# Performance work log

Hardware: AMD Instinct MI355X
Metric: run time of the kernel (lower is better)

## Reference

```python
import jax, jax.numpy as jnp
import numpy as np

FACTOR = 2
DIM = 3
F3 = FACTOR ** DIM            # 8
B = 2                          # batch size
S = 128                        # cubic spatial shape (spatial_shape = [S, S, S])
N = 262144                     # number of active voxels
C = 32                         # feature channels
MAXS = (S + FACTOR - 1) // FACTOR  # 64, downsampled grid extent per dim
# OFFSET per torch code: cumprod of MAX reversed, reversed, + [1]
OFFSET = (MAXS ** 3, MAXS ** 2, MAXS, 1)


def setup_inputs() -> dict:
    rng = np.random.default_rng(0)
    # unique voxel coords: sample N distinct cells from the B x S^3 grid
    lin = rng.permutation(B * S ** 3)[:N].astype(np.int64)
    b = lin // (S ** 3)
    r = lin % (S ** 3)
    x = r // (S * S)
    y = (r // S) % S
    z = r % S
    coords = jnp.asarray(np.stack([b, x, y, z], axis=-1), dtype=jnp.int32)  # [N, 4]
    feats = jax.random.normal(jax.random.key(0), (N, C), dtype=jnp.float32)
    return {"feats": feats, "coords": coords}


def reference(feats, coords):
    c = coords.astype(jnp.int32)
    down = c[:, 1:] // FACTOR          # [N, 3] downsampled spatial coords
    sub = c[:, 1:] % FACTOR            # [N, 3] position within factor^3 cell
    # subidx = sum(sub[..., i] * factor**i), i=0 -> x
    subidx = sub[:, 0] + sub[:, 1] * FACTOR + sub[:, 2] * (FACTOR ** 2)
    # linear code over (batch, dx, dy, dz)
    code = (c[:, 0] * OFFSET[0] + down[:, 0] * OFFSET[1]
            + down[:, 1] * OFFSET[2] + down[:, 2] * OFFSET[3])
    # unique with static size=N (M_unique <= N); pad with out-of-range sentinel
    code_u, idx = jnp.unique(code, return_inverse=True, size=N,
                             fill_value=B * MAXS ** 3)
    idx = idx.reshape(-1)
    new_coords = jnp.stack(
        [code_u // OFFSET[0]]
        + [(code_u // OFFSET[i + 1]) % MAXS for i in range(DIM)], axis=-1)
    # scatter feats into channel-expanded buffer; padded rows stay zero
    buf = jnp.zeros((N * F3, C), dtype=feats.dtype).at[idx * F3 + subidx].set(feats)
    new_feats = buf.reshape(N, F3 * C)   # [N_pad, factor^3 * C]
    return new_feats, new_coords
```

## Files before the change

### kernel.cpp

```cpp
#include <hip/hip_runtime.h>

typedef unsigned int u32;
typedef float __attribute__((ext_vector_type(4))) f4;
typedef unsigned int __attribute__((ext_vector_type(4))) u4;

static constexpr u32 NCODES = 524288u;
static constexpr u32 ZB = 1024u;
static constexpr u32 TAG = 0xFFFFFFFFu;

__device__ __forceinline__ u32 code_of(int4 c) {
  return ((u32)c.x << 18) + ((u32)(c.y >> 1) << 12) +
         ((u32)(c.z >> 1) << 6) + (u32)(c.w >> 1);
}

__device__ __forceinline__ void zero_n(f4* __restrict__ base, u32 zb, u32 t, u32 cnt) {
  const f4 z = {0.f, 0.f, 0.f, 0.f};
  for (u32 i = zb * 256u + t; i < cnt; i += ZB * 256u)
    __builtin_nontemporal_store(z, base + i);
}

__global__ void k_1(const int4* __restrict__ coords, u32* __restrict__ mark, u32 n,
                    f4* __restrict__ outc4, f4* __restrict__ zbase, u32 zcnt) {
  u32 b = blockIdx.x, t = threadIdx.x;
  u32 mb = n / 256u, sb = n / 1024u;
  if (b < mb) {
    mark[code_of(coords[b * 256u + t])] = TAG;
  } else if (b < mb + sb) {
    u32 i = (b - mb) * 256u + t;
    const f4 s4 = {2.f, 0.f, 0.f, 0.f};
    u32 span = sb * 256u;
    for (u32 k = 0; k < 4u; ++k)
      __builtin_nontemporal_store(s4, outc4 + i + k * span);
  } else {
    zero_n(zbase, b - mb - sb, t, zcnt);
  }
}

__global__ void k_2(const u4* __restrict__ mark, u32* __restrict__ bsum,
                    f4* __restrict__ zbase, u32 zcnt) {
  u32 b = blockIdx.x, t = threadIdx.x;
  if (b >= 512u) { zero_n(zbase, b - 512u, t, zcnt); return; }
  u4 m = mark[b * 256u + t];
  u32 s = (m.x == TAG) + (m.y == TAG) + (m.z == TAG) + (m.w == TAG);
  for (int d = 32; d > 0; d >>= 1) s += __shfl_down(s, d, 64);
  __shared__ u32 ws4[4];
  if ((t & 63u) == 0u) ws4[t >> 6] = s;
  __syncthreads();
  if (t == 0) bsum[b] = ws4[0] + ws4[1] + ws4[2] + ws4[3];
}

__device__ __forceinline__ void wrc(float* __restrict__ outc, u32 r, u32 code) {
  f4 p = {(float)(code >> 18), (float)((code >> 12) & 63u),
          (float)((code >> 6) & 63u), (float)(code & 63u)};
  __builtin_nontemporal_store(p, (f4*)outc + r);
}

__global__ void k_3(u32* __restrict__ codes, const u32* __restrict__ bsum,
                    float* __restrict__ outc, f4* __restrict__ zbase, u32 zcnt) {
  u32 b = blockIdx.x, t = threadIdx.x;
  if (b >= 512u) { zero_n(zbase, b - 512u, t, zcnt); return; }

  u32 v0 = bsum[t], v1 = bsum[t + 256u];
  u32 s = (t < b ? v0 : 0u) + (t + 256u < b ? v1 : 0u);
  for (int d = 32; d > 0; d >>= 1) s += __shfl_down(s, d, 64);
  __shared__ u32 ws4[4];
  if ((t & 63u) == 0u) ws4[t >> 6] = s;
  __syncthreads();
  u32 boff = ws4[0] + ws4[1] + ws4[2] + ws4[3];

  u4 m = ((const u4*)codes)[b * 256u + t];
  u32 p0 = (m.x == TAG), p1 = (m.y == TAG), p2 = (m.z == TAG), p3 = (m.w == TAG);
  u32 tsum = p0 + p1 + p2 + p3;
  u32 incl = tsum;
  u32 lane = t & 63u;
  for (int d = 1; d < 64; d <<= 1) {
    u32 v = __shfl_up(incl, d, 64);
    if (lane >= (u32)d) incl += v;
  }
  __shared__ u32 wsum[4];
  if (lane == 63u) wsum[t >> 6] = incl;
  __syncthreads();
  u32 woff = boff;
  for (u32 w = 0; w < (t >> 6); ++w) woff += wsum[w];
  u32 e0 = woff + incl - tsum;
  u32 e1 = e0 + p0, e2 = e1 + p1, e3 = e2 + p2;
  u4 r = {e0, e1, e2, e3};
  ((u4*)codes)[b * 256u + t] = r;
  u32 base = b * 1024u + t * 4u;
  if (p0) wrc(outc, e0, base + 0u);
  if (p1) wrc(outc, e1, base + 1u);
  if (p2) wrc(outc, e2, base + 2u);
  if (p3) wrc(outc, e3, base + 3u);
}

__global__ void k_4(const f4* __restrict__ feats, const int4* __restrict__ coords,
                    const u32* __restrict__ rank, f4* __restrict__ out, u32 n8) {
  u32 tid = blockIdx.x * 256u + threadIdx.x;
  if (tid >= n8) return;
  u32 row = tid >> 3, q = tid & 7u;
  int4 c = coords[row];
  u32 code = code_of(c);
  u32 sub = (u32)(c.y & 1) + ((u32)(c.z & 1) << 1) + ((u32)(c.w & 1) << 2);
  f4 f = __builtin_nontemporal_load(feats + tid);
  __builtin_nontemporal_store(f, out + ((size_t)rank[code] * 8u + sub) * 8u + q);
}

extern "C" void kernel_launch(void* const* d_in, const int* in_sizes, int n_in,
                              void* d_out, int out_size, void* d_ws, size_t ws_size,
                              hipStream_t stream) {
  const float* feats = (const float*)d_in[0];
  const int* coords  = (const int*)d_in[1];
  u32 n = (u32)(in_sizes[1] / 4);
  f4* out4 = (f4*)d_out;
  float* outc = (float*)d_out + (size_t)n * 256u;

  u32* codes = (u32*)d_ws;
  u32* bsum  = codes + NCODES;

  u32 feats4 = n * 64u;
  u32 c1 = feats4 / 3u;
  u32 c2 = c1;
  u32 c3 = feats4 - 2u * c1;
  u32 mb = n / 256u, sb = n / 1024u;

  k_1<<<mb + sb + ZB, 256, 0, stream>>>((const int4*)coords, codes, n,
                                        (f4*)outc, out4, c1);
  k_2<<<512u + ZB, 256, 0, stream>>>((const u4*)codes, bsum, out4 + c1, c2);
  k_3<<<512u + ZB, 256, 0, stream>>>(codes, bsum, outc, out4 + c1 + c2, c3);
  k_4<<<(n * 8u) / 256u, 256, 0, stream>>>((const f4*)feats, (const int4*)coords,
                                           codes, out4, n * 8u);
}
```

Measured before the change: 318.0 us.

## Fuse the four pipeline kernels into one cooperative kernel with grid syncs

Replaces the four separate launches (mark, block count, scan/emit coords, scatter) with a single cooperative kernel. Inside it, grid.sync() separates the phases, and the output zero-fill is split into thirds interleaved with the first three phases. The aim is to remove kernel launch gaps and tail effects between stages. In exchange, the grid is limited to 1024 resident blocks with grid-stride loops, and each phase now pays a grid-wide barrier. The launch also depends on every block being co-resident under the 4-blocks-per-CU bound.

```diff
diff --git a/kernel.cpp b/kernel.cpp
--- a/kernel.cpp
+++ b/kernel.cpp
@@ -1,11 +1,13 @@
 #include <hip/hip_runtime.h>
+#include <hip/hip_cooperative_groups.h>
+
+namespace cg = cooperative_groups;
 
 typedef unsigned int u32;
 typedef float __attribute__((ext_vector_type(4))) f4;
 typedef unsigned int __attribute__((ext_vector_type(4))) u4;
 
 static constexpr u32 NCODES = 524288u;
-static constexpr u32 ZB = 1024u;
 static constexpr u32 TAG = 0xFFFFFFFFu;
 
 __device__ __forceinline__ u32 code_of(int4 c) {
@@ -13,120 +15,114 @@
          ((u32)(c.z >> 1) << 6) + (u32)(c.w >> 1);
 }
 
-__device__ __forceinline__ void zero_n(f4* __restrict__ base, u32 zb, u32 t, u32 cnt) {
+__device__ __forceinline__ void zero_span(f4* __restrict__ base, u32 lo, u32 hi,
+                                          u32 gtid, u32 gt) {
   const f4 z = {0.f, 0.f, 0.f, 0.f};
-  for (u32 i = zb * 256u + t; i < cnt; i += ZB * 256u)
+  for (u32 i = lo + gtid; i < hi; i += gt)
     __builtin_nontemporal_store(z, base + i);
 }
 
-__global__ void k_1(const int4* __restrict__ coords, u32* __restrict__ mark, u32 n,
-                    f4* __restrict__ outc4, f4* __restrict__ zbase, u32 zcnt) {
+__global__ __launch_bounds__(256, 4)
+void k_all(const int4* __restrict__ coords, const f4* __restrict__ feats,
+           f4* __restrict__ out4, u32* __restrict__ codes, u32* __restrict__ bsum,
+           u32 n) {
+  cg::grid_group grid = cg::this_grid();
   u32 b = blockIdx.x, t = threadIdx.x;
-  u32 mb = n / 256u, sb = n / 1024u;
-  if (b < mb) {
-    mark[code_of(coords[b * 256u + t])] = TAG;
-  } else if (b < mb + sb) {
-    u32 i = (b - mb) * 256u + t;
-    const f4 s4 = {2.f, 0.f, 0.f, 0.f};
-    u32 span = sb * 256u;
-    for (u32 k = 0; k < 4u; ++k)
-      __builtin_nontemporal_store(s4, outc4 + i + k * span);
-  } else {
-    zero_n(zbase, b - mb - sb, t, zcnt);
+  u32 gt = gridDim.x * 256u, gtid = b * 256u + t;
+  f4* outc4 = out4 + (size_t)n * 64u;
+  u32 total4 = n * 64u;
+  u32 zc = total4 / 3u;
+
+  __shared__ u32 ws4[4];
+  __shared__ u32 wsum[4];
+
+  for (u32 i = gtid; i < n; i += gt)
+    codes[code_of(coords[i])] = TAG;
+  const f4 s4 = {2.f, 0.f, 0.f, 0.f};
+  for (u32 i = gtid; i < n; i += gt)
+    __builtin_nontemporal_store(s4, outc4 + i);
+  zero_span(out4, 0u, zc, gtid, gt);
+  grid.sync();
+
+  if (b < 512u) {
+    u4 m = ((const u4*)codes)[b * 256u + t];
+    u32 s = (m.x == TAG) + (m.y == TAG) + (m.z == TAG) + (m.w == TAG);
+    for (int d = 32; d > 0; d >>= 1) s += __shfl_down(s, d, 64);
+    if ((t & 63u) == 0u) ws4[t >> 6] = s;
+    __syncthreads();
+    if (t == 0) bsum[b] = ws4[0] + ws4[1] + ws4[2] + ws4[3];
   }
-}
+  zero_span(out4, zc, 2u * zc, gtid, gt);
+  grid.sync();
 
-__global__ void k_2(const u4* __restrict__ mark, u32* __restrict__ bsum,
-                    f4* __restrict__ zbase, u32 zcnt) {
-  u32 b = blockIdx.x, t = threadIdx.x;
-  if (b >= 512u) { zero_n(zbase, b - 512u, t, zcnt); return; }
-  u4 m = mark[b * 256u + t];
-  u32 s = (m.x == TAG) + (m.y == TAG) + (m.z == TAG) + (m.w == TAG);
-  for (int d = 32; d > 0; d >>= 1) s += __shfl_down(s, d, 64);
-  __shared__ u32 ws4[4];
-  if ((t & 63u) == 0u) ws4[t >> 6] = s;
-  __syncthreads();
-  if (t == 0) bsum[b] = ws4[0] + ws4[1] + ws4[2] + ws4[3];
-}
+  if (b < 512u) {
+    u32 v0 = bsum[t], v1 = bsum[t + 256u];
+    u32 s = (t < b ? v0 : 0u) + (t + 256u < b ? v1 : 0u);
+    for (int d = 32; d > 0; d >>= 1) s += __shfl_down(s, d, 64);
+    if ((t & 63u) == 0u) ws4[t >> 6] = s;
+    __syncthreads();
+    u32 boff = ws4[0] + ws4[1] + ws4[2] + ws4[3];
 
-__device__ __forceinline__ void wrc(float* __restrict__ outc, u32 r, u32 code) {
-  f4 p = {(float)(code >> 18), (float)((code >> 12) & 63u),
-          (float)((code >> 6) & 63u), (float)(code & 63u)};
-  __builtin_nontemporal_store(p, (f4*)outc + r);
-}
+    u4 m = ((const u4*)codes)[b * 256u + t];
+    u32 p0 = (m.x == TAG), p1 = (m.y == TAG), p2 = (m.z == TAG), p3 = (m.w == TAG);
+    u32 tsum = p0 + p1 + p2 + p3;
+    u32 incl = tsum;
+    u32 lane = t & 63u;
+    for (int d = 1; d < 64; d <<= 1) {
+      u32 v = __shfl_up(incl, d, 64);
+      if (lane >= (u32)d) incl += v;
+    }
+    if (lane == 63u) wsum[t >> 6] = incl;
+    __syncthreads();
+    u32 woff = boff;
+    for (u32 w = 0; w < (t >> 6); ++w) woff += wsum[w];
+    u32 e0 = woff + incl - tsum;
+    u32 e1 = e0 + p0, e2 = e1 + p1, e3 = e2 + p2;
+    u4 r = {e0, e1, e2, e3};
+    ((u4*)codes)[b * 256u + t] = r;
+    u32 base = b * 1024u + t * 4u;
+    if (p0) { f4 p = {(float)(base >> 18), (float)(((base + 0u) >> 12) & 63u),
+                      (float)(((base + 0u) >> 6) & 63u), (float)((base + 0u) & 63u)};
+              __builtin_nontemporal_store(p, outc4 + e0); }
+    if (p1) { u32 cd = base + 1u;
+              f4 p = {(float)(cd >> 18), (float)((cd >> 12) & 63u),
+                      (float)((cd >> 6) & 63u), (float)(cd & 63u)};
+              __builtin_nontemporal_store(p, outc4 + e1); }
+    if (p2) { u32 cd = base + 2u;
+              f4 p = {(float)(cd >> 18), (float)((cd >> 12) & 63u),
+                      (float)((cd >> 6) & 63u), (float)(cd & 63u)};
+              __builtin_nontemporal_store(p, outc4 + e2); }
+    if (p3) { u32 cd = base + 3u;
+              f4 p = {(float)(cd >> 18), (float)((cd >> 12) & 63u),
+                      (float)((cd >> 6) & 63u), (float)(cd & 63u)};
+              __builtin_nontemporal_store(p, outc4 + e3); }
+  }
+  zero_span(out4, 2u * zc, total4, gtid, gt);
+  grid.sync();
 
-__global__ void k_3(u32* __restrict__ codes, const u32* __restrict__ bsum,
-                    float* __restrict__ outc, f4* __restrict__ zbase, u32 zcnt) {
-  u32 b = blockIdx.x, t = threadIdx.x;
-  if (b >= 512u) { zero_n(zbase, b - 512u, t, zcnt); return; }
-
-  u32 v0 = bsum[t], v1 = bsum[t + 256u];
-  u32 s = (t < b ? v0 : 0u) + (t + 256u < b ? v1 : 0u);
-  for (int d = 32; d > 0; d >>= 1) s += __shfl_down(s, d, 64);
-  __shared__ u32 ws4[4];
-  if ((t & 63u) == 0u) ws4[t >> 6] = s;
-  __syncthreads();
-  u32 boff = ws4[0] + ws4[1] + ws4[2] + ws4[3];
-
-  u4 m = ((const u4*)codes)[b * 256u + t];
-  u32 p0 = (m.x == TAG), p1 = (m.y == TAG), p2 = (m.z == TAG), p3 = (m.w == TAG);
-  u32 tsum = p0 + p1 + p2 + p3;
-  u32 incl = tsum;
-  u32 lane = t & 63u;
-  for (int d = 1; d < 64; d <<= 1) {
-    u32 v = __shfl_up(incl, d, 64);
-    if (lane >= (u32)d) incl += v;
+  u32 n8 = n * 8u;
+  for (u32 i = gtid; i < n8; i += gt) {
+    u32 row = i >> 3, q = i & 7u;
+    int4 c = coords[row];
+    u32 code = code_of(c);
+    u32 sub = (u32)(c.y & 1) + ((u32)(c.z & 1) << 1) + ((u32)(c.w & 1) << 2);
+    f4 f = __builtin_nontemporal_load(feats + i);
+    __builtin_nontemporal_store(f, out4 + ((size_t)codes[code] * 8u + sub) * 8u + q);
   }
-  __shared__ u32 wsum[4];
-  if (lane == 63u) wsum[t >> 6] = incl;
-  __syncthreads();
-  u32 woff = boff;
-  for (u32 w = 0; w < (t >> 6); ++w) woff += wsum[w];
-  u32 e0 = woff + incl - tsum;
-  u32 e1 = e0 + p0, e2 = e1 + p1, e3 = e2 + p2;
-  u4 r = {e0, e1, e2, e3};
-  ((u4*)codes)[b * 256u + t] = r;
-  u32 base = b * 1024u + t * 4u;
-  if (p0) wrc(outc, e0, base + 0u);
-  if (p1) wrc(outc, e1, base + 1u);
-  if (p2) wrc(outc, e2, base + 2u);
-  if (p3) wrc(outc, e3, base + 3u);
-}
-
-__global__ void k_4(const f4* __restrict__ feats, const int4* __restrict__ coords,
-                    const u32* __restrict__ rank, f4* __restrict__ out, u32 n8) {
-  u32 tid = blockIdx.x * 256u + threadIdx.x;
-  if (tid >= n8) return;
-  u32 row = tid >> 3, q = tid & 7u;
-  int4 c = coords[row];
-  u32 code = code_of(c);
-  u32 sub = (u32)(c.y & 1) + ((u32)(c.z & 1) << 1) + ((u32)(c.w & 1) << 2);
-  f4 f = __builtin_nontemporal_load(feats + tid);
-  __builtin_nontemporal_store(f, out + ((size_t)rank[code] * 8u + sub) * 8u + q);
 }
 
 extern "C" void kernel_launch(void* const* d_in, const int* in_sizes, int n_in,
                               void* d_out, int out_size, void* d_ws, size_t ws_size,
                               hipStream_t stream) {
-  const float* feats = (const float*)d_in[0];
-  const int* coords  = (const int*)d_in[1];
+  const int4* coords = (const int4*)d_in[1];
+  const f4* feats    = (const f4*)d_in[0];
   u32 n = (u32)(in_sizes[1] / 4);
   f4* out4 = (f4*)d_out;
-  float* outc = (float*)d_out + (size_t)n * 256u;
 
   u32* codes = (u32*)d_ws;
   u32* bsum  = codes + NCODES;
 
-  u32 feats4 = n * 64u;
-  u32 c1 = feats4 / 3u;
-  u32 c2 = c1;
-  u32 c3 = feats4 - 2u * c1;
-  u32 mb = n / 256u, sb = n / 1024u;
-
-  k_1<<<mb + sb + ZB, 256, 0, stream>>>((const int4*)coords, codes, n,
-                                        (f4*)outc, out4, c1);
-  k_2<<<512u + ZB, 256, 0, stream>>>((const u4*)codes, bsum, out4 + c1, c2);
-  k_3<<<512u + ZB, 256, 0, stream>>>(codes, bsum, outc, out4 + c1 + c2, c3);
-  k_4<<<(n * 8u) / 256u, 256, 0, stream>>>((const f4*)feats, (const int4*)coords,
-                                           codes, out4, n * 8u);
+  void* args[] = {(void*)&coords, (void*)&feats, (void*)&out4,
+                  (void*)&codes, (void*)&bsum, (void*)&n};
+  hipLaunchCooperativeKernel((void*)k_all, dim3(1024), dim3(256), args, 0, stream);
 }
```

Result: slower. 727.7 us (+128.8%).
